# Performance work log

Hardware: AMD Instinct MI355X
Metric: run time of the kernel (lower is better)

The kernel has to match this reference:

```python
import jax, jax.numpy as jnp
import numpy as np
from jax import lax

EPS = 1e-12  # torch F.normalize eps


def _l2norm(x):
    n = jnp.linalg.norm(x, axis=-1, keepdims=True)
    return x / jnp.maximum(n, EPS)


def _conv1x1(x, w):
    # x: [B,C,H,W], w: [O,C] (1x1 conv, no bias)
    return jnp.einsum('bchw,oc->bohw', x, w)


def _se(x, w1, w2):
    # AdaptiveAvgPool2d(1) -> 1x1 conv (no bias) -> ReLU -> 1x1 conv (no bias) -> ReLU
    p = jnp.mean(x, axis=(2, 3))                      # [B,256]
    h = jax.nn.relu(jnp.einsum('bc,oc->bo', p, w1))   # [B,320]
    return jax.nn.relu(jnp.einsum('bc,oc->bo', h, w2))  # [B,1280]


def _tdec(x, wk_w, wk_b, wv_w, wv_b, red_w, rise_w, rise_b):
    # fc_reduce: 1x1 conv 256->128
    x1 = _conv1x1(x, red_w)                           # [B,128,H,W]
    B, d, H, W = x1.shape
    t = x1.reshape(B, d, H * W).transpose(0, 2, 1)    # [B,N,128] tokens
    # same WK linear produces both q and k (xq == xk in the source)
    k = _l2norm(jnp.einsum('bnd,ed->bne', t, wk_w) + wk_b)  # [B,N,128]
    v = _l2norm(jnp.einsum('bnd,ed->bne', t, wv_w) + wv_b)  # [B,N,128]
    # bmm(wq[B,d,N], wk[B,N,d]) -> [B,d,d] channel gram, temp 30 softmax
    attn = jax.nn.softmax(jnp.einsum('bni,bnj->bij', k, k) * 30.0, axis=-1)
    # bmm(attn[B,d,d], v^T[B,d,N]) -> [B,d,N], reshape back to map
    ot = jnp.einsum('bij,bnj->bin', attn, v).reshape(B, d, H, W)
    return _conv1x1(ot, rise_w) + rise_b[None, :, None, None]


def _fwd(x0, x1, x2, x3, x4, spec_w1, spec_w2, comm_w1, comm_w2,
         pre_w, pre_b, wk1_w, wk1_b, wv1_w, wv1_b, red1_w, rise1_w, rise1_b,
         wk2_w, wk2_b, wv2_w, wv2_b, red2_w, rise2_w, rise2_b):
    xs = jnp.stack([x0, x1, x2, x3, x4])              # [5,B,256,H,W]
    B = x0.shape[0]
    # reduce(lambda x,y: abs(x-y), down_x)
    diff = x0
    for xi in (x1, x2, x3, x4):
        diff = jnp.abs(diff - xi)
    ssum = xs.sum(axis=0)
    wd = jax.nn.softmax(_se(diff, spec_w1, spec_w2).reshape(B, 5, 256), axis=1)
    ws = jax.nn.softmax(_se(ssum, comm_w1, comm_w2).reshape(B, 5, 256), axis=1)
    # v2[i] = x_i*wd_i + x_i*ws_i + x_i ; v3 = sum_i v2[i]
    v3 = jnp.einsum('sbchw,bsc->bchw', xs, wd + ws + 1.0)
    pre = jax.nn.relu(
        lax.conv_general_dilated(v3, pre_w, (1, 1), ((1, 1), (1, 1)),
                                 dimension_numbers=('NCHW', 'OIHW', 'NCHW'))
        + pre_b[None, :, None, None])
    f1 = _tdec(pre, wk1_w, wk1_b, wv1_w, wv1_b, red1_w, rise1_w, rise1_b)
    f3 = _tdec(f1 + v3, wk2_w, wk2_b, wv2_w, wv2_b, red2_w, rise2_w, rise2_b)
    return f1 + f3 + v3


def setup_inputs() -> dict:
    key = jax.random.key(0)
    ks = iter(jax.random.split(key, 40))
    B, C, H, W = 16, 256, 64, 64

    def p(shape, scale=0.05):
        return jax.random.normal(next(ks), shape, jnp.float32) * scale

    inp = {f'x{i}': jax.random.normal(next(ks), (B, C, H, W), jnp.float32) for i in range(5)}
    inp.update(
        spec_w1=p((320, 256)), spec_w2=p((1280, 320)),
        comm_w1=p((320, 256)), comm_w2=p((1280, 320)),
        pre_w=p((256, 256, 3, 3)), pre_b=p((256,)),
        wk1_w=p((128, 128)), wk1_b=p((128,)), wv1_w=p((128, 128)), wv1_b=p((128,)),
        red1_w=p((128, 256)), rise1_w=p((256, 128)), rise1_b=p((256,)),
        wk2_w=p((128, 128)), wk2_b=p((128,)), wv2_w=p((128, 128)), wv2_b=p((128,)),
        red2_w=p((128, 256)), rise2_w=p((256, 128)), rise2_b=p((256,)),
    )
    return inp


def reference(x0, x1, x2, x3, x4, spec_w1, spec_w2, comm_w1, comm_w2,
              pre_w, pre_b, wk1_w, wk1_b, wv1_w, wv1_b, red1_w, rise1_w, rise1_b,
              wk2_w, wk2_b, wv2_w, wv2_b, red2_w, rise2_w, rise2_b):
    return _fwd(x0, x1, x2, x3, x4, spec_w1, spec_w2, comm_w1, comm_w2,
                pre_w, pre_b, wk1_w, wk1_b, wv1_w, wv1_b, red1_w, rise1_w, rise1_b,
                wk2_w, wk2_b, wv2_w, wv2_b, red2_w, rise2_w, rise2_b)
```

## Files before the change

kernel.cpp:

```cpp
#include <hip/hip_runtime.h>

#define DI __device__ __forceinline__

typedef short s16x8 __attribute__((ext_vector_type(8)));
typedef unsigned short u16;
typedef u16 u16x8 __attribute__((ext_vector_type(8)));
typedef u16 u16x16 __attribute__((ext_vector_type(16)));
typedef float f32x4 __attribute__((ext_vector_type(4)));

DI float bf2f(u16 v) { return __builtin_bit_cast(float, (unsigned)v << 16); }
DI u16 f2bf(float f) {
  unsigned u = __builtin_bit_cast(unsigned, f);
  return (u16)((u + 0x7fffu + ((u >> 16) & 1u)) >> 16);
}

__global__ void k_cast8(u16* __restrict__ dst,
    const float* __restrict__ s0, const float* __restrict__ s1,
    const float* __restrict__ s2, const float* __restrict__ s3,
    const float* __restrict__ s4, const float* __restrict__ s5,
    const float* __restrict__ s6, const float* __restrict__ s7) {
  int i = blockIdx.x * 256 + threadIdx.x;
  const float* src; int base;
  if (i < 32768) { src = s0; base = 0; }
  else if (i < 49152) { src = s1; base = 32768; }
  else if (i < 65536) { src = s2; base = 49152; }
  else if (i < 98304) { src = s3; base = 65536; }
  else if (i < 131072) { src = s4; base = 98304; }
  else if (i < 147456) { src = s5; base = 131072; }
  else if (i < 163840) { src = s6; base = 147456; }
  else { src = s7; base = 163840; }
  dst[i] = f2bf(src[i - base]);
}

__global__ void k_wconv(u16* __restrict__ dst, const float* __restrict__ src) {
  int i = blockIdx.x * 256 + threadIdx.x;
  if (i < 9 * 256 * 256) {
    int tap = i >> 16, rem = i & 65535;
    dst[i] = f2bf(src[(size_t)rem * 9 + tap]);
  }
}

__global__ __launch_bounds__(256) void k_pool(
    const float* __restrict__ x0, const float* __restrict__ x1,
    const float* __restrict__ x2, const float* __restrict__ x3,
    const float* __restrict__ x4, float* __restrict__ pd, float* __restrict__ ps) {
  int c = blockIdx.x, b = blockIdx.y;
  size_t base = ((size_t)b * 256 + c) * 4096;
  float sd = 0.f, sm = 0.f;
  for (int p = threadIdx.x; p < 4096; p += 256) {
    float a0 = x0[base + p], a1 = x1[base + p], a2 = x2[base + p];
    float a3 = x3[base + p], a4 = x4[base + p];
    float d = fabsf(a0 - a1); d = fabsf(d - a2); d = fabsf(d - a3); d = fabsf(d - a4);
    sd += d; sm += a0 + a1 + a2 + a3 + a4;
  }
  for (int o = 32; o; o >>= 1) { sd += __shfl_xor(sd, o); sm += __shfl_xor(sm, o); }
  __shared__ float rb[4][2];
  int wv = threadIdx.x >> 6, lane = threadIdx.x & 63;
  if (!lane) { rb[wv][0] = sd; rb[wv][1] = sm; }
  __syncthreads();
  if (!threadIdx.x) {
    float a = rb[0][0] + rb[1][0] + rb[2][0] + rb[3][0];
    float s2 = rb[0][1] + rb[1][1] + rb[2][1] + rb[3][1];
    pd[b * 256 + c] = a * (1.f / 4096.f);
    ps[b * 256 + c] = s2 * (1.f / 4096.f);
  }
}

__global__ __launch_bounds__(256) void k_se1(
    const float* __restrict__ pd, const float* __restrict__ ps,
    const float* __restrict__ sw1, const float* __restrict__ cw1,
    float* __restrict__ h1) {
  int b = blockIdx.y, z = blockIdx.z;
  int wv = threadIdx.x >> 6, lane = threadIdx.x & 63;
  int e = blockIdx.x * 4 + wv;
  const float* in = (z ? ps : pd) + b * 256;
  const float* w = (z ? cw1 : sw1) + (size_t)e * 256;
  float a = 0.f;
#pragma unroll
  for (int i = 0; i < 4; ++i) a += in[lane + 64 * i] * w[lane + 64 * i];
  for (int o = 32; o; o >>= 1) a += __shfl_xor(a, o);
  if (!lane) h1[((size_t)z * 16 + b) * 320 + e] = fmaxf(a, 0.f);
}

__global__ __launch_bounds__(256) void k_se2(
    const float* __restrict__ h1, const float* __restrict__ sw2,
    const float* __restrict__ cw2, float* __restrict__ h2) {
  int b = blockIdx.y, z = blockIdx.z;
  int wv = threadIdx.x >> 6, lane = threadIdx.x & 63;
  int e = blockIdx.x * 4 + wv;
  const float* in = h1 + ((size_t)z * 16 + b) * 320;
  const float* w = (z ? cw2 : sw2) + (size_t)e * 320;
  float a = 0.f;
#pragma unroll
  for (int i = 0; i < 5; ++i) a += in[lane + 64 * i] * w[lane + 64 * i];
  for (int o = 32; o; o >>= 1) a += __shfl_xor(a, o);
  if (!lane) h2[((size_t)z * 16 + b) * 1280 + e] = fmaxf(a, 0.f);
}

__global__ __launch_bounds__(256) void k_se3(
    const float* __restrict__ h2, float* __restrict__ wt) {
  int b = blockIdx.x, t = threadIdx.x;
  const float* Hs = h2 + (size_t)b * 1280;
  const float* Hc = h2 + (size_t)(16 + b) * 1280;
  float d0 = Hs[t], d1 = Hs[256 + t], d2 = Hs[512 + t], d3 = Hs[768 + t], d4 = Hs[1024 + t];
  float m = fmaxf(fmaxf(fmaxf(d0, d1), fmaxf(d2, d3)), d4);
  float e0 = expf(d0 - m), e1 = expf(d1 - m), e2 = expf(d2 - m), e3 = expf(d3 - m), e4 = expf(d4 - m);
  float inv = 1.f / (e0 + e1 + e2 + e3 + e4);
  float c0 = Hc[t], c1 = Hc[256 + t], c2 = Hc[512 + t], c3 = Hc[768 + t], c4 = Hc[1024 + t];
  float mc = fmaxf(fmaxf(fmaxf(c0, c1), fmaxf(c2, c3)), c4);
  float g0 = expf(c0 - mc), g1 = expf(c1 - mc), g2 = expf(c2 - mc), g3 = expf(c3 - mc), g4 = expf(c4 - mc);
  float ci = 1.f / (g0 + g1 + g2 + g3 + g4);
  size_t base = (size_t)b * 1280 + t;
  wt[base + 0 * 256] = e0 * inv + g0 * ci + 1.f;
  wt[base + 1 * 256] = e1 * inv + g1 * ci + 1.f;
  wt[base + 2 * 256] = e2 * inv + g2 * ci + 1.f;
  wt[base + 3 * 256] = e3 * inv + g3 * ci + 1.f;
  wt[base + 4 * 256] = e4 * inv + g4 * ci + 1.f;
}

__global__ __launch_bounds__(256) void k_v3(
    const float* __restrict__ x0, const float* __restrict__ x1,
    const float* __restrict__ x2, const float* __restrict__ x3,
    const float* __restrict__ x4, const float* __restrict__ wt,
    u16* __restrict__ v3b) {
  int h = blockIdx.x, b = blockIdx.y;
  __shared__ float W[1280];
  __shared__ u16 T[256][72];
  int t = threadIdx.x, wv = t >> 6, l = t & 63;
  for (int s = t; s < 1280; s += 256) W[s] = wt[(size_t)b * 1280 + s];
  __syncthreads();
  size_t rowbase = (size_t)b * 256 * 4096 + h * 64 + l;
#pragma unroll 4
  for (int k = 0; k < 64; ++k) {
    int c = wv * 64 + k;
    size_t a = rowbase + (size_t)c * 4096;
    float s = x0[a] * W[c] + x1[a] * W[256 + c] + x2[a] * W[512 + c] +
              x3[a] * W[768 + c] + x4[a] * W[1024 + c];
    T[c][l] = f2bf(s);
  }
  __syncthreads();
  int w = t >> 2, oct = t & 3;
  size_t obase = ((size_t)b * 4096 + h * 64 + w) * 256;
  for (int pass = 0; pass < 8; ++pass) {
    int c0 = oct * 8 + pass * 32;
    u16x8 ov;
#pragma unroll
    for (int jj = 0; jj < 8; ++jj) ov[jj] = T[c0 + jj][w];
    *(u16x8*)(v3b + obase + c0) = ov;
  }
}

__global__ __launch_bounds__(256) void k_conv(
    const u16* __restrict__ v3b, const u16* __restrict__ Wt,
    const float* __restrict__ bias, u16* __restrict__ pre) {
  int o = blockIdx.x;
  int wg = (o & 7) * 128 + (o >> 3);
  int oh = wg & 1, hp = (wg >> 1) & 31, b = wg >> 6;
  __shared__ __align__(16) u16 Ain[4 * 66 * 40];
  __shared__ __align__(16) u16 Bld[2][128 * 40];
  int t = threadIdx.x, wv = t >> 6, lane = t & 63;
  int wm = (wv >> 1) * 64, wn = (wv & 1) * 64, fr = lane & 15, ko = lane >> 4;

  auto loadA = [&](int cc, int s) -> u16x16 {
    int r = s >> 7, rest = s & 127, w = rest >> 1, half = rest & 1;
    int hs = hp * 2 - 1 + r;
    u16x16 v = {};
    if ((unsigned)hs < 64u)
      v = *(const u16x16*)(v3b + (((size_t)b * 64 + hs) * 64 + w) * 256 + cc * 32 + half * 16);
    return v;
  };
  auto storeA = [&](int s, u16x16 v) {
    int r = s >> 7, rest = s & 127, w = rest >> 1, half = rest & 1;
    *(u16x16*)(Ain + (r * 66 + w + 1) * 40 + half * 16) = v;
  };
  auto loadB = [&](int tap, int cc) -> u16x16 {
    int n = t >> 1, half = t & 1;
    return *(const u16x16*)(Wt + ((size_t)tap * 256 + oh * 128 + n) * 256 + cc * 32 + half * 16);
  };
  auto storeB = [&](int bsel, u16x16 v) {
    int n = t >> 1, half = t & 1;
    *(u16x16*)(Bld[bsel] + n * 40 + half * 16) = v;
  };

  for (int s = t; s < 320; s += 256) {
    int r = s / 80, rem = s % 80;
    int col = (rem >= 40) ? 65 : 0, c = rem % 40;
    Ain[(r * 66 + col) * 40 + c] = 0;
  }
  storeA(t, loadA(0, t));
  storeA(t + 256, loadA(0, t + 256));
  storeB(0, loadB(0, 0));
  __syncthreads();

  f32x4 acc[4][4] = {};
  int buf = 0;
  for (int cc = 0; cc < 8; ++cc) {
#pragma unroll
    for (int tap = 0; tap < 9; ++tap) {
      u16x16 pA0, pA1, pB;
      bool doA = false, doB = false;
      if (tap < 8) {
        doB = true;
        pB = loadB(tap + 1, cc);
      } else if (cc < 7) {
        doA = true; doB = true;
        pB = loadB(0, cc + 1);
        pA0 = loadA(cc + 1, t);
        pA1 = loadA(cc + 1, t + 256);
      }
      const int dh = tap / 3 - 1, dw = tap % 3 - 1;
      s16x8 af[4], bfr[4];
#pragma unroll
      for (int i = 0; i < 4; ++i) {
        int m = wm + i * 16 + fr, r = m >> 6, wq = m & 63;
        af[i] = *(const s16x8*)(Ain + ((r + dh + 1) * 66 + (wq + dw + 1)) * 40 + ko * 8);
      }
#pragma unroll
      for (int j = 0; j < 4; ++j)
        bfr[j] = *(const s16x8*)(Bld[buf] + (wn + j * 16 + fr) * 40 + ko * 8);
#pragma unroll
      for (int i = 0; i < 4; ++i)
#pragma unroll
        for (int j = 0; j < 4; ++j)
          acc[i][j] = __builtin_amdgcn_mfma_f32_16x16x32_bf16(af[i], bfr[j], acc[i][j], 0, 0, 0);
      if (doA) __syncthreads();
      if (doB) storeB(buf ^ 1, pB);
      if (doA) { storeA(t, pA0); storeA(t + 256, pA1); }
      __syncthreads();
      buf ^= 1;
    }
  }
#pragma unroll
  for (int i = 0; i < 4; ++i) {
    int m0 = wm + i * 16 + ko * 4;
#pragma unroll
    for (int j = 0; j < 4; ++j) {
      int och = oh * 128 + wn + j * 16 + fr;
      float bv = bias[och];
#pragma unroll
      for (int r = 0; r < 4; ++r) {
        float v = fmaxf(acc[i][j][r] + bv, 0.f);
        pre[((size_t)b * 4096 + hp * 128 + m0 + r) * 256 + och] = f2bf(v);
      }
    }
  }
}

__global__ __launch_bounds__(256) void k_qkv(
    const u16* __restrict__ in,
    const u16* __restrict__ redW,
    const u16* __restrict__ wkW,
    const u16* __restrict__ wvW,
    const float* __restrict__ kb, const float* __restrict__ vb,
    u16* __restrict__ vout,
    u16* __restrict__ khat) {
  int nt = blockIdx.x, b = blockIdx.y;
  const u16* Ab = in + ((size_t)b * 4096 + nt * 128) * 256;
  __shared__ __align__(16) u16 Ald[128 * 40];
  __shared__ __align__(16) u16 Bld[128 * 40];
  __shared__ __align__(16) u16 T[128 * 136];
  __shared__ float SS[2][128];
  int t = threadIdx.x, wv = t >> 6, lane = t & 63;
  int wm = (wv >> 1) * 64, wn = (wv & 1) * 64, fr = lane & 15, ko = lane >> 4;
  f32x4 acc[4][4] = {};
  for (int kc = 0; kc < 256; kc += 32) {
    for (int s = t; s < 512; s += 256) {
      int r = s >> 2, ks = s & 3;
      *(u16x8*)(Ald + r * 40 + ks * 8) = *(const u16x8*)(Ab + (size_t)r * 256 + kc + ks * 8);
    }
    for (int s = t; s < 512; s += 256) {
      int r = s >> 2, ks = s & 3;
      *(u16x8*)(Bld + r * 40 + ks * 8) = *(const u16x8*)(redW + (size_t)r * 256 + kc + ks * 8);
    }
    __syncthreads();
    s16x8 af[4], bf[4];
#pragma unroll
    for (int i = 0; i < 4; ++i) af[i] = *(const s16x8*)(Ald + (wm + i * 16 + fr) * 40 + ko * 8);
#pragma unroll
    for (int j = 0; j < 4; ++j) bf[j] = *(const s16x8*)(Bld + (wn + j * 16 + fr) * 40 + ko * 8);
#pragma unroll
    for (int i = 0; i < 4; ++i)
#pragma unroll
      for (int j = 0; j < 4; ++j)
        acc[i][j] = __builtin_amdgcn_mfma_f32_16x16x32_bf16(af[i], bf[j], acc[i][j], 0, 0, 0);
    __syncthreads();
  }
#pragma unroll
  for (int i = 0; i < 4; ++i)
#pragma unroll
    for (int j = 0; j < 4; ++j)
#pragma unroll
      for (int r = 0; r < 4; ++r)
        T[(wm + i * 16 + ko * 4 + r) * 136 + wn + j * 16 + fr] = f2bf(acc[i][j][r]);

  for (int z = 0; z < 2; ++z) {
    const u16* W = z ? wkW : wvW;
    const float* bias = z ? kb : vb;
    f32x4 a2[4][4] = {};
#pragma unroll
    for (int h = 0; h < 2; ++h) {
      __syncthreads();
      for (int s = t; s < 512; s += 256) {
        int r = s >> 2, ks = s & 3;
        *(u16x8*)(Ald + r * 40 + ks * 8) = *(const u16x8*)(W + (size_t)r * 128 + h * 64 + ks * 8);
      }
      for (int s = t; s < 512; s += 256) {
        int r = s >> 2, ks = s & 3;
        *(u16x8*)(Bld + r * 40 + ks * 8) = *(const u16x8*)(W + (size_t)r * 128 + h * 64 + 32 + ks * 8);
      }
      __syncthreads();
#pragma unroll
      for (int kk = 0; kk < 2; ++kk) {
        const u16* Bsrc = kk ? Bld : Ald;
        s16x8 af[4], bf[4];
#pragma unroll
        for (int i = 0; i < 4; ++i)
          af[i] = *(const s16x8*)(T + (size_t)(wm + i * 16 + fr) * 136 + h * 64 + kk * 32 + ko * 8);
#pragma unroll
        for (int j = 0; j < 4; ++j)
          bf[j] = *(const s16x8*)(Bsrc + (wn + j * 16 + fr) * 40 + ko * 8);
#pragma unroll
        for (int i = 0; i < 4; ++i)
#pragma unroll
          for (int j = 0; j < 4; ++j)
            a2[i][j] = __builtin_amdgcn_mfma_f32_16x16x32_bf16(af[i], bf[j], a2[i][j], 0, 0, 0);
      }
    }
    float bj[4];
#pragma unroll
    for (int j = 0; j < 4; ++j) bj[j] = bias[wn + j * 16 + fr];
    float pss[4][4];
#pragma unroll
    for (int i = 0; i < 4; ++i)
#pragma unroll
      for (int r = 0; r < 4; ++r) pss[i][r] = 0.f;
#pragma unroll
    for (int i = 0; i < 4; ++i)
#pragma unroll
      for (int j = 0; j < 4; ++j)
#pragma unroll
        for (int r = 0; r < 4; ++r) {
          float v = a2[i][j][r] + bj[j];
          a2[i][j][r] = v;
          pss[i][r] += v * v;
        }
#pragma unroll
    for (int m = 1; m < 16; m <<= 1)
#pragma unroll
      for (int i = 0; i < 4; ++i)
#pragma unroll
        for (int r = 0; r < 4; ++r) pss[i][r] += __shfl_xor(pss[i][r], m);
    if (fr == 0)
#pragma unroll
      for (int i = 0; i < 4; ++i)
#pragma unroll
        for (int r = 0; r < 4; ++r) SS[wv & 1][wm + i * 16 + ko * 4 + r] = pss[i][r];
    __syncthreads();
    float sc[4][4];
#pragma unroll
    for (int i = 0; i < 4; ++i)
#pragma unroll
      for (int r = 0; r < 4; ++r) {
        int tok = wm + i * 16 + ko * 4 + r;
        float s2 = SS[0][tok] + SS[1][tok];
        sc[i][r] = 1.f / fmaxf(sqrtf(s2), 1e-12f);
      }
#pragma unroll
    for (int i = 0; i < 4; ++i)
#pragma unroll
      for (int j = 0; j < 4; ++j)
#pragma unroll
        for (int r = 0; r < 4; ++r) a2[i][j][r] *= sc[i][r];
    if (z == 0) {
      size_t tokbase = (size_t)b * 4096 + nt * 128;
#pragma unroll
      for (int i = 0; i < 4; ++i)
#pragma unroll
        for (int j = 0; j < 4; ++j) {
          u16* dst = vout + (tokbase + wm + i * 16 + ko * 4) * 128 + wn + j * 16 + fr;
#pragma unroll
          for (int r = 0; r < 4; ++r) dst[(size_t)r * 128] = f2bf(a2[i][j][r]);
        }
    } else {
#pragma unroll
      for (int i = 0; i < 4; ++i)
#pragma unroll
        for (int j = 0; j < 4; ++j)
#pragma unroll
          for (int r = 0; r < 4; ++r)
            T[(size_t)(wn + j * 16 + fr) * 136 + wm + i * 16 + ko * 4 + r] = f2bf(a2[i][j][r]);
      __syncthreads();
      for (int s = t; s < 2048; s += 256) {
        int ch = s >> 4, sg = s & 15;
        *(u16x8*)(khat + ((size_t)b * 128 + ch) * 4096 + nt * 128 + sg * 8) =
            *(const u16x8*)(T + ch * 136 + sg * 8);
      }
    }
  }
}

template <int MODE>
__global__ __launch_bounds__(256) void k_gemm(
    const u16* __restrict__ A, int lda, const u16* __restrict__ B0,
    const u16* __restrict__ B1, int ldb, int K,
    const float* __restrict__ bias0, const float* __restrict__ bias1,
    u16* __restrict__ out0, u16* __restrict__ out1,
    const u16* __restrict__ add0, const u16* __restrict__ add1,
    float* __restrict__ outf) {
  int nt = blockIdx.x, b = blockIdx.y, z = blockIdx.z;
  const u16* Ab = A + ((size_t)b * 4096 + nt * 128) * (size_t)lda;
  const u16* Bb;
  if constexpr (MODE == 2) Bb = B0 + (size_t)b * 128 * ldb;
  else Bb = B0 + (size_t)z * 128 * ldb;
  __shared__ __align__(16) u16 Ald[128 * 40];
  __shared__ __align__(16) u16 Bld[128 * 40];
  int t = threadIdx.x, wv = t >> 6, lane = t & 63;
  int wm = (wv >> 1) * 64, wn = (wv & 1) * 64, fr = lane & 15, ko = lane >> 4;
  f32x4 acc[4][4] = {};
  for (int kc = 0; kc < K; kc += 32) {
    for (int s = t; s < 512; s += 256) {
      int r = s >> 2, ks = s & 3;
      *(u16x8*)(Ald + r * 40 + ks * 8) = *(const u16x8*)(Ab + (size_t)r * lda + kc + ks * 8);
    }
    for (int s = t; s < 512; s += 256) {
      int r = s >> 2, ks = s & 3;
      *(u16x8*)(Bld + r * 40 + ks * 8) = *(const u16x8*)(Bb + (size_t)r * ldb + kc + ks * 8);
    }
    __syncthreads();
    s16x8 af[4], bf[4];
#pragma unroll
    for (int i = 0; i < 4; ++i) af[i] = *(const s16x8*)(Ald + (wm + i * 16 + fr) * 40 + ko * 8);
#pragma unroll
    for (int j = 0; j < 4; ++j) bf[j] = *(const s16x8*)(Bld + (wn + j * 16 + fr) * 40 + ko * 8);
#pragma unroll
    for (int i = 0; i < 4; ++i)
#pragma unroll
      for (int j = 0; j < 4; ++j)
        acc[i][j] = __builtin_amdgcn_mfma_f32_16x16x32_bf16(af[i], bf[j], acc[i][j], 0, 0, 0);
    __syncthreads();
  }
  size_t tokbase = (size_t)b * 4096 + nt * 128;
#pragma unroll
  for (int i = 0; i < 4; ++i) {
    int m0 = wm + i * 16 + ko * 4;
#pragma unroll
    for (int j = 0; j < 4; ++j) {
      int nc = wn + j * 16 + fr;
      if constexpr (MODE == 2) {
        u16* dst = out0 + (tokbase + m0) * 128 + nc;
#pragma unroll
        for (int r = 0; r < 4; ++r) dst[(size_t)r * 128] = f2bf(acc[i][j][r]);
      } else if constexpr (MODE == 3) {
        int o = z * 128 + nc;
        float bv = bias0[o];
        size_t idx = (tokbase + m0) * 256 + o;
#pragma unroll
        for (int r = 0; r < 4; ++r) {
          float f1v = acc[i][j][r] + bv;
          out0[idx + (size_t)r * 256] = f2bf(f1v);
          out1[idx + (size_t)r * 256] = f2bf(f1v + bf2f(add0[idx + (size_t)r * 256]));
        }
      } else {
        int o = z * 128 + nc;
        float bv = bias0[o];
        size_t idx = (tokbase + m0) * 256 + o;
        f32x4 vv;
#pragma unroll
        for (int r = 0; r < 4; ++r)
          vv[r] = acc[i][j][r] + bv + bf2f(add0[idx + (size_t)r * 256]) + bf2f(add1[idx + (size_t)r * 256]);
        *(f32x4*)(outf + ((size_t)b * 256 + o) * 4096 + nt * 128 + m0) = vv;
      }
    }
  }
}

__global__ __launch_bounds__(256) void k_gram(const u16* __restrict__ kt, float* __restrict__ gp) {
  int ks = blockIdx.x, b = blockIdx.y;
  const u16* base = kt + (size_t)b * 128 * 4096 + ks * 256;
  __shared__ __align__(16) u16 Tld[128 * 40];
  int t = threadIdx.x, wv = t >> 6, lane = t & 63;
  int wm = (wv >> 1) * 64, wn = (wv & 1) * 64, fr = lane & 15, ko = lane >> 4;
  f32x4 acc[4][4] = {};
  for (int kc = 0; kc < 256; kc += 32) {
    for (int s = t; s < 512; s += 256) {
      int r = s >> 2, k2 = s & 3;
      *(u16x8*)(Tld + r * 40 + k2 * 8) = *(const u16x8*)(base + (size_t)r * 4096 + kc + k2 * 8);
    }
    __syncthreads();
    s16x8 af[4], bf[4];
#pragma unroll
    for (int i = 0; i < 4; ++i) af[i] = *(const s16x8*)(Tld + (wm + i * 16 + fr) * 40 + ko * 8);
#pragma unroll
    for (int j = 0; j < 4; ++j) bf[j] = *(const s16x8*)(Tld + (wn + j * 16 + fr) * 40 + ko * 8);
#pragma unroll
    for (int i = 0; i < 4; ++i)
#pragma unroll
      for (int j = 0; j < 4; ++j)
        acc[i][j] = __builtin_amdgcn_mfma_f32_16x16x32_bf16(af[i], bf[j], acc[i][j], 0, 0, 0);
    __syncthreads();
  }
  float* dst = gp + ((size_t)(ks * 16 + b) * 128) * 128;
#pragma unroll
  for (int i = 0; i < 4; ++i) {
    int m0 = wm + i * 16 + ko * 4;
#pragma unroll
    for (int j = 0; j < 4; ++j) {
      int nc = wn + j * 16 + fr;
#pragma unroll
      for (int r = 0; r < 4; ++r) dst[(size_t)(m0 + r) * 128 + nc] = acc[i][j][r];
    }
  }
}

__global__ void k_soft(const float* __restrict__ gp, u16* __restrict__ attn) {
  int i = blockIdx.x, b = blockIdx.y, l = threadIdx.x;
  float s0 = 0.f, s1 = 0.f;
  for (int ks = 0; ks < 16; ++ks) {
    const float* row = gp + (((size_t)ks * 16 + b) * 128 + i) * 128;
    s0 += row[l]; s1 += row[l + 64];
  }
  s0 *= 30.f; s1 *= 30.f;
  float m = fmaxf(s0, s1);
  for (int o = 32; o; o >>= 1) m = fmaxf(m, __shfl_xor(m, o));
  float e0 = expf(s0 - m), e1 = expf(s1 - m);
  float s = e0 + e1;
  for (int o = 32; o; o >>= 1) s += __shfl_xor(s, o);
  float inv = 1.f / s;
  u16* dst = attn + ((size_t)b * 128 + i) * 128;
  dst[l] = f2bf(e0 * inv);
  dst[l + 64] = f2bf(e1 * inv);
}

extern "C" void kernel_launch(void* const* d_in, const int* in_sizes, int n_in,
                              void* d_out, int out_size, void* d_ws, size_t ws_size,
                              hipStream_t stream) {
  (void)in_sizes; (void)n_in; (void)out_size; (void)ws_size;
  const float* x0 = (const float*)d_in[0];
  const float* x1 = (const float*)d_in[1];
  const float* x2 = (const float*)d_in[2];
  const float* x3 = (const float*)d_in[3];
  const float* x4 = (const float*)d_in[4];
  const float* spec_w1 = (const float*)d_in[5];
  const float* spec_w2 = (const float*)d_in[6];
  const float* comm_w1 = (const float*)d_in[7];
  const float* comm_w2 = (const float*)d_in[8];
  const float* pre_w = (const float*)d_in[9];
  const float* pre_bias = (const float*)d_in[10];
  const float* wk1_w = (const float*)d_in[11];
  const float* wk1_b = (const float*)d_in[12];
  const float* wv1_w = (const float*)d_in[13];
  const float* wv1_b = (const float*)d_in[14];
  const float* red1_w = (const float*)d_in[15];
  const float* rise1_w = (const float*)d_in[16];
  const float* rise1_b = (const float*)d_in[17];
  const float* wk2_w = (const float*)d_in[18];
  const float* wk2_b = (const float*)d_in[19];
  const float* wv2_w = (const float*)d_in[20];
  const float* wv2_b = (const float*)d_in[21];
  const float* red2_w = (const float*)d_in[22];
  const float* rise2_w = (const float*)d_in[23];
  const float* rise2_b = (const float*)d_in[24];
  float* out = (float*)d_out;

  char* wsp = (char*)d_ws;
  size_t off = 0;
  auto alloc = [&](size_t bytes) -> void* {
    off = (off + 255) & ~(size_t)255;
    void* p = wsp + off;
    off += bytes;
    return p;
  };
  float* pd = (float*)alloc(16 * 256 * 4);
  float* ps = (float*)alloc(16 * 256 * 4);
  float* h1b = (float*)alloc(2 * 16 * 320 * 4);
  float* h2b = (float*)alloc(2 * 16 * 1280 * 4);
  float* wtb = (float*)alloc(16 * 5 * 256 * 4);
  u16* v3b = (u16*)alloc((size_t)16 * 4096 * 256 * 2);
  u16* Wtc = (u16*)alloc((size_t)9 * 256 * 256 * 2);
  u16* wall = (u16*)alloc((size_t)196608 * 2);
  u16* red1b = wall;
  u16* wk1b = wall + 32768;
  u16* wv1b = wall + 49152;
  u16* rise1b = wall + 65536;
  u16* red2b = wall + 98304;
  u16* wk2b = wall + 131072;
  u16* wv2b = wall + 147456;
  u16* rise2b = wall + 163840;
  u16* pre = (u16*)alloc((size_t)16 * 4096 * 256 * 2);
  u16* tbuf = (u16*)alloc((size_t)16 * 4096 * 128 * 2);
  u16* khat = (u16*)alloc((size_t)16 * 4096 * 128 * 2);
  u16* vbuf = (u16*)alloc((size_t)16 * 4096 * 128 * 2);
  u16* attn = (u16*)alloc((size_t)16 * 128 * 128 * 2);
  u16* Obuf = (u16*)alloc((size_t)16 * 4096 * 128 * 2);
  u16* f1b = (u16*)alloc((size_t)16 * 4096 * 256 * 2);
  float* gpart = (float*)tbuf;
  u16* in2b = pre;

  k_cast8<<<dim3(768), 256, 0, stream>>>(wall, red1_w, wk1_w, wv1_w, rise1_w,
                                         red2_w, wk2_w, wv2_w, rise2_w);
  k_wconv<<<dim3(2304), 256, 0, stream>>>(Wtc, pre_w);

  k_pool<<<dim3(256, 16), 256, 0, stream>>>(x0, x1, x2, x3, x4, pd, ps);
  k_se1<<<dim3(80, 16, 2), 256, 0, stream>>>(pd, ps, spec_w1, comm_w1, h1b);
  k_se2<<<dim3(320, 16, 2), 256, 0, stream>>>(h1b, spec_w2, comm_w2, h2b);
  k_se3<<<dim3(16), 256, 0, stream>>>(h2b, wtb);
  k_v3<<<dim3(64, 16), 256, 0, stream>>>(x0, x1, x2, x3, x4, wtb, v3b);
  k_conv<<<dim3(1024), 256, 0, stream>>>(v3b, Wtc, pre_bias, pre);

  k_qkv<<<dim3(32, 16), 256, 0, stream>>>(pre, red1b, wk1b, wv1b, wk1_b, wv1_b, vbuf, khat);
  k_gram<<<dim3(16, 16), 256, 0, stream>>>(khat, gpart);
  k_soft<<<dim3(128, 16), 64, 0, stream>>>(gpart, attn);
  k_gemm<2><<<dim3(32, 16, 1), 256, 0, stream>>>(vbuf, 128, attn, nullptr, 128, 128,
      nullptr, nullptr, Obuf, nullptr, nullptr, nullptr, nullptr);
  k_gemm<3><<<dim3(32, 16, 2), 256, 0, stream>>>(Obuf, 128, rise1b, nullptr, 128, 128,
      rise1_b, nullptr, f1b, in2b, v3b, nullptr, nullptr);

  k_qkv<<<dim3(32, 16), 256, 0, stream>>>(in2b, red2b, wk2b, wv2b, wk2_b, wv2_b, vbuf, khat);
  k_gram<<<dim3(16, 16), 256, 0, stream>>>(khat, gpart);
  k_soft<<<dim3(128, 16), 64, 0, stream>>>(gpart, attn);
  k_gemm<2><<<dim3(32, 16, 1), 256, 0, stream>>>(vbuf, 128, attn, nullptr, 128, 128,
      nullptr, nullptr, Obuf, nullptr, nullptr, nullptr, nullptr);
  k_gemm<4><<<dim3(32, 16, 2), 256, 0, stream>>>(Obuf, 128, rise2b, nullptr, 128, 128,
      rise2_b, nullptr, nullptr, nullptr, f1b, v3b, out);
}
```

Baseline: 494.5 us.

## Prefetch conv weights two steps ahead with single LDS buffer; vectorize pooling loads

```diff
diff --git a/kernel.cpp b/kernel.cpp
--- a/kernel.cpp
+++ b/kernel.cpp
@@ -47,11 +47,17 @@
   int c = blockIdx.x, b = blockIdx.y;
   size_t base = ((size_t)b * 256 + c) * 4096;
   float sd = 0.f, sm = 0.f;
-  for (int p = threadIdx.x; p < 4096; p += 256) {
-    float a0 = x0[base + p], a1 = x1[base + p], a2 = x2[base + p];
-    float a3 = x3[base + p], a4 = x4[base + p];
-    float d = fabsf(a0 - a1); d = fabsf(d - a2); d = fabsf(d - a3); d = fabsf(d - a4);
-    sd += d; sm += a0 + a1 + a2 + a3 + a4;
+  for (int p4 = threadIdx.x; p4 < 1024; p4 += 256) {
+    f32x4 a0 = *(const f32x4*)(x0 + base + p4 * 4);
+    f32x4 a1 = *(const f32x4*)(x1 + base + p4 * 4);
+    f32x4 a2 = *(const f32x4*)(x2 + base + p4 * 4);
+    f32x4 a3 = *(const f32x4*)(x3 + base + p4 * 4);
+    f32x4 a4 = *(const f32x4*)(x4 + base + p4 * 4);
+#pragma unroll
+    for (int e = 0; e < 4; ++e) {
+      float d = fabsf(a0[e] - a1[e]); d = fabsf(d - a2[e]); d = fabsf(d - a3[e]); d = fabsf(d - a4[e]);
+      sd += d; sm += a0[e] + a1[e] + a2[e] + a3[e] + a4[e];
+    }
   }
   for (int o = 32; o; o >>= 1) { sd += __shfl_xor(sd, o); sm += __shfl_xor(sm, o); }
   __shared__ float rb[4][2];
@@ -157,7 +163,7 @@
   int wg = (o & 7) * 128 + (o >> 3);
   int oh = wg & 1, hp = (wg >> 1) & 31, b = wg >> 6;
   __shared__ __align__(16) u16 Ain[4 * 66 * 40];
-  __shared__ __align__(16) u16 Bld[2][128 * 40];
+  __shared__ __align__(16) u16 Bls[128 * 40];
   int t = threadIdx.x, wv = t >> 6, lane = t & 63;
   int wm = (wv >> 1) * 64, wn = (wv & 1) * 64, fr = lane & 15, ko = lane >> 4;
 
@@ -177,9 +183,9 @@
     int n = t >> 1, half = t & 1;
     return *(const u16x16*)(Wt + ((size_t)tap * 256 + oh * 128 + n) * 256 + cc * 32 + half * 16);
   };
-  auto storeB = [&](int bsel, u16x16 v) {
+  auto storeB = [&](u16x16 v) {
     int n = t >> 1, half = t & 1;
-    *(u16x16*)(Bld[bsel] + n * 40 + half * 16) = v;
+    *(u16x16*)(Bls + n * 40 + half * 16) = v;
   };
 
   for (int s = t; s < 320; s += 256) {
@@ -187,27 +193,16 @@
     int col = (rem >= 40) ? 65 : 0, c = rem % 40;
     Ain[(r * 66 + col) * 40 + c] = 0;
   }
-  storeA(t, loadA(0, t));
-  storeA(t + 256, loadA(0, t + 256));
-  storeB(0, loadB(0, 0));
+  u16x16 pA0 = loadA(0, t), pA1 = loadA(0, t + 256);
+  u16x16 rB = loadB(0, 0);
+  storeA(t, pA0); storeA(t + 256, pA1); storeB(rB);
+  rB = loadB(1, 0);
   __syncthreads();
 
   f32x4 acc[4][4] = {};
-  int buf = 0;
   for (int cc = 0; cc < 8; ++cc) {
 #pragma unroll
     for (int tap = 0; tap < 9; ++tap) {
-      u16x16 pA0, pA1, pB;
-      bool doA = false, doB = false;
-      if (tap < 8) {
-        doB = true;
-        pB = loadB(tap + 1, cc);
-      } else if (cc < 7) {
-        doA = true; doB = true;
-        pB = loadB(0, cc + 1);
-        pA0 = loadA(cc + 1, t);
-        pA1 = loadA(cc + 1, t + 256);
-      }
       const int dh = tap / 3 - 1, dw = tap % 3 - 1;
       s16x8 af[4], bfr[4];
 #pragma unroll
@@ -217,17 +212,24 @@
       }
 #pragma unroll
       for (int j = 0; j < 4; ++j)
-        bfr[j] = *(const s16x8*)(Bld[buf] + (wn + j * 16 + fr) * 40 + ko * 8);
+        bfr[j] = *(const s16x8*)(Bls + (wn + j * 16 + fr) * 40 + ko * 8);
 #pragma unroll
       for (int i = 0; i < 4; ++i)
 #pragma unroll
         for (int j = 0; j < 4; ++j)
           acc[i][j] = __builtin_amdgcn_mfma_f32_16x16x32_bf16(af[i], bfr[j], acc[i][j], 0, 0, 0);
-      if (doA) __syncthreads();
-      if (doB) storeB(buf ^ 1, pB);
-      if (doA) { storeA(t, pA0); storeA(t + 256, pA1); }
-      __syncthreads();
-      buf ^= 1;
+      const int u = cc * 9 + tap;
+      if (u < 71) {
+        __syncthreads();
+        storeB(rB);
+        if (tap == 8) { storeA(t, pA0); storeA(t + 256, pA1); }
+        if (u + 2 <= 71) {
+          const int un = u + 2, tn = un % 9, cn = un / 9;
+          rB = loadB(tn, cn);
+        }
+        if (tap == 7 && cc < 7) { pA0 = loadA(cc + 1, t); pA1 = loadA(cc + 1, t + 256); }
+        __syncthreads();
+      }
     }
   }
 #pragma unroll
```

After: 477.9 us. 1.03x faster.
